# Optimization experiments

Measured on AMD Instinct MI355X. Metric: run time of the kernel, lower is better.

## Reference

```python
import jax, jax.numpy as jnp
import numpy as np

B, L, D = 16, 4096, 1024          # batch, query (latent) length, latent_dim
MODS = [("image", 2048), ("audio", 1024), ("text", 768)]


def setup_inputs() -> dict:
    key = jax.random.key(0)
    ks = iter(jax.random.split(key, 64))
    inp = {"S": jax.random.normal(next(ks), (B, L, D), jnp.float32)}
    for mod, din in MODS:
        inp[f"feat_{mod}"] = jax.random.normal(next(ks), (B, din), jnp.float32)
        # kv_proj: Linear(input_dim -> latent_dim)
        inp[f"Wkv_{mod}"] = jax.random.normal(next(ks), (D, din), jnp.float32) * (din ** -0.5)
        inp[f"bkv_{mod}"] = jnp.zeros((D,), jnp.float32)
        # MHA value projection (D -> D); k/q projections drop out because
        # softmax over a single key is identically 1 (exact, not approximate).
        inp[f"Wv_{mod}"] = jax.random.normal(next(ks), (D, D), jnp.float32) * (D ** -0.5)
        inp[f"bv_{mod}"] = jnp.zeros((D,), jnp.float32)
        # MHA out_proj (D -> D)
        inp[f"Wo_{mod}"] = jax.random.normal(next(ks), (D, D), jnp.float32) * (D ** -0.5)
        inp[f"bo_{mod}"] = jnp.zeros((D,), jnp.float32)
    return inp


def _modality_out(feat, Wkv, bkv, Wv, bv, Wo, bo):
    # kv_proj -> v_proj -> out_proj ; attention weights over 1 key are exactly 1,
    # so the MHA output is this vector broadcast over all L query positions.
    kv = feat @ Wkv.T + bkv        # [B, D]
    v = kv @ Wv.T + bv             # [B, D]
    return v @ Wo.T + bo           # [B, D]


def reference(S,
              feat_image, Wkv_image, bkv_image, Wv_image, bv_image, Wo_image, bo_image,
              feat_audio, Wkv_audio, bkv_audio, Wv_audio, bv_audio, Wo_audio, bo_audio,
              feat_text, Wkv_text, bkv_text, Wv_text, bv_text, Wo_text, bo_text):
    # Sequential residual adds S = S + out_mod commute; fuse into one add.
    delta = (_modality_out(feat_image, Wkv_image, bkv_image, Wv_image, bv_image, Wo_image, bo_image)
             + _modality_out(feat_audio, Wkv_audio, bkv_audio, Wv_audio, bv_audio, Wo_audio, bo_audio)
             + _modality_out(feat_text, Wkv_text, bkv_text, Wv_text, bv_text, Wo_text, bo_text))
    return S + delta[:, None, :]   # broadcast over query length L
```

## Files before the change

### kernel.cpp

```cpp
#include <hip/hip_runtime.h>


#define B_ 16
#define L_ 4096
#define D_ 1024

__global__ void gemv64(const float* __restrict__ x,
                       const float* __restrict__ W,
                       const float* __restrict__ bias,
                       float* __restrict__ y,
                       int K, int accumulate) {
    int wave = (blockIdx.x * blockDim.x + threadIdx.x) >> 6;
    int lane = threadIdx.x & 63;
    int b = wave >> 10;
    int d = wave & 1023;

    const float* xr = x + (size_t)b * K;
    const float* wr = W + (size_t)d * K;

    float sum = 0.f;
    for (int k = lane * 4; k < K; k += 256) {
        float4 xv = *(const float4*)(xr + k);
        float4 wv = *(const float4*)(wr + k);
        sum += xv.x * wv.x + xv.y * wv.y + xv.z * wv.z + xv.w * wv.w;
    }
    for (int off = 32; off; off >>= 1)
        sum += __shfl_xor(sum, off, 64);

    if (lane == 0) {
        float r = sum + bias[d];
        if (accumulate) y[wave] += r;
        else            y[wave]  = r;
    }
}

__global__ void add_bcast(const float4* __restrict__ S,
                          const float4* __restrict__ delta,
                          float4* __restrict__ out) {
    int i = blockIdx.x * blockDim.x + threadIdx.x;
    int b  = i >> 20;
    int d4 = i & 255;
    float4 s = S[i];
    float4 dl = delta[(b << 8) + d4];
    float4 r;
    r.x = s.x + dl.x;
    r.y = s.y + dl.y;
    r.z = s.z + dl.z;
    r.w = s.w + dl.w;
    out[i] = r;
}

extern "C" void kernel_launch(void* const* d_in, const int* in_sizes, int n_in,
                              void* d_out, int out_size, void* d_ws, size_t ws_size,
                              hipStream_t stream) {
    const float* S = (const float*)d_in[0];

    const int dins[3] = {2048, 1024, 768};
    const float *feat[3], *Wkv[3], *bkv[3], *Wv[3], *bv[3], *Wo[3], *bo[3];
    for (int m = 0; m < 3; ++m) {
        int base = 1 + m * 7;
        feat[m] = (const float*)d_in[base + 0];
        Wkv[m]  = (const float*)d_in[base + 1];
        bkv[m]  = (const float*)d_in[base + 2];
        Wv[m]   = (const float*)d_in[base + 3];
        bv[m]   = (const float*)d_in[base + 4];
        Wo[m]   = (const float*)d_in[base + 5];
        bo[m]   = (const float*)d_in[base + 6];
    }

    float* ws = (float*)d_ws;
    const int BD = B_ * D_;
    float* kv[3]  = {ws, ws + BD, ws + 2 * BD};
    float* v[3]   = {ws + 3 * BD, ws + 4 * BD, ws + 5 * BD};
    float* delta  = ws + 6 * BD;

    const int gemv_blocks = (BD * 64) / 256;
    const dim3 gb(gemv_blocks), tb(256);

    for (int m = 0; m < 3; ++m)
        gemv64<<<gb, tb, 0, stream>>>(feat[m], Wkv[m], bkv[m], kv[m], dins[m], 0);
    for (int m = 0; m < 3; ++m)
        gemv64<<<gb, tb, 0, stream>>>(kv[m], Wv[m], bv[m], v[m], D_, 0);
    for (int m = 0; m < 3; ++m)
        gemv64<<<gb, tb, 0, stream>>>(v[m], Wo[m], bo[m], delta, D_, m != 0);

    const int total4 = (B_ * L_ * D_) / 4;
    add_bcast<<<total4 / 256, 256, 0, stream>>>((const float4*)S,
                                                (const float4*)delta,
                                                (float4*)d_out);
}
```

Before: 545.7 us.

## Batch per-modality GEMVs into one launch per stage and stream the broadcast add

The three per-modality GEMVs of each stage are merged into a single launch indexed by modality, and the out-projection stage sums all three modalities inside one wave, so the read-modify-write accumulation into delta goes away. This cuts ten launches down to four. The broadcast add becomes a grid-stride loop with nontemporal loads and stores, meant to keep the streaming S traffic out of the cache. The total is dominated by the 256MB read plus 256MB write of S, so the achievable gain is limited to launch overhead and small GEMV costs.

```diff
diff --git a/kernel.cpp b/kernel.cpp
--- a/kernel.cpp
+++ b/kernel.cpp
@@ -5,18 +5,27 @@
 #define L_ 4096
 #define D_ 1024
 
-__global__ void gemv64(const float* __restrict__ x,
-                       const float* __restrict__ W,
-                       const float* __restrict__ bias,
-                       float* __restrict__ y,
-                       int K, int accumulate) {
-    int wave = (blockIdx.x * blockDim.x + threadIdx.x) >> 6;
+typedef float v4f __attribute__((ext_vector_type(4)));
+
+struct StageArgs {
+    const float* x[3];
+    const float* W[3];
+    const float* bias[3];
+    float*       y[3];
+    int          K[3];
+};
+
+__global__ __launch_bounds__(256) void gemv_stage(StageArgs a) {
+    int wid  = (blockIdx.x * 256 + threadIdx.x) >> 6;
     int lane = threadIdx.x & 63;
-    int b = wave >> 10;
-    int d = wave & 1023;
+    int m = wid >> 14;
+    int r = wid & 16383;
+    int bb = r >> 10;
+    int d  = r & 1023;
+    int K = a.K[m];
 
-    const float* xr = x + (size_t)b * K;
-    const float* wr = W + (size_t)d * K;
+    const float* xr = a.x[m] + bb * K;
+    const float* wr = a.W[m] + (size_t)d * K;
 
     float sum = 0.f;
     for (int k = lane * 4; k < K; k += 256) {
@@ -24,30 +33,56 @@
         float4 wv = *(const float4*)(wr + k);
         sum += xv.x * wv.x + xv.y * wv.y + xv.z * wv.z + xv.w * wv.w;
     }
-    for (int off = 32; off; off >>= 1)
-        sum += __shfl_xor(sum, off, 64);
+    for (int off = 32; off; off >>= 1) sum += __shfl_xor(sum, off, 64);
 
-    if (lane == 0) {
-        float r = sum + bias[d];
-        if (accumulate) y[wave] += r;
-        else            y[wave]  = r;
-    }
+    if (lane == 0) a.y[m][(bb << 10) + d] = sum + a.bias[m][d];
 }
 
-__global__ void add_bcast(const float4* __restrict__ S,
-                          const float4* __restrict__ delta,
-                          float4* __restrict__ out) {
-    int i = blockIdx.x * blockDim.x + threadIdx.x;
-    int b  = i >> 20;
-    int d4 = i & 255;
-    float4 s = S[i];
-    float4 dl = delta[(b << 8) + d4];
-    float4 r;
-    r.x = s.x + dl.x;
-    r.y = s.y + dl.y;
-    r.z = s.z + dl.z;
-    r.w = s.w + dl.w;
-    out[i] = r;
+struct Stage3Args {
+    const float* v0; const float* v1; const float* v2;
+    const float* W0; const float* W1; const float* W2;
+    const float* b0; const float* b1; const float* b2;
+    float* delta;
+};
+
+__global__ __launch_bounds__(256) void gemv_stage3(Stage3Args a) {
+    int wid  = (blockIdx.x * 256 + threadIdx.x) >> 6;
+    int lane = threadIdx.x & 63;
+    int bb = wid >> 10;
+    int d  = wid & 1023;
+
+    const float* xs[3] = { a.v0 + (bb << 10), a.v1 + (bb << 10), a.v2 + (bb << 10) };
+    const float* ws[3] = { a.W0 + ((size_t)d << 10), a.W1 + ((size_t)d << 10),
+                           a.W2 + ((size_t)d << 10) };
+    float sum = 0.f;
+    #pragma unroll
+    for (int m = 0; m < 3; ++m) {
+        const float* xr = xs[m];
+        const float* wr = ws[m];
+        #pragma unroll
+        for (int k = lane * 4; k < 1024; k += 256) {
+            float4 xv = *(const float4*)(xr + k);
+            float4 wv = *(const float4*)(wr + k);
+            sum += xv.x * wv.x + xv.y * wv.y + xv.z * wv.z + xv.w * wv.w;
+        }
+    }
+    for (int off = 32; off; off >>= 1) sum += __shfl_xor(sum, off, 64);
+
+    if (lane == 0)
+        a.delta[(bb << 10) + d] = sum + a.b0[d] + a.b1[d] + a.b2[d];
+}
+
+__global__ __launch_bounds__(256) void add_bcast(const v4f* __restrict__ S,
+                                                 const v4f* __restrict__ delta,
+                                                 v4f* __restrict__ out, int total4) {
+    int stride = gridDim.x * 256;
+    for (int i = blockIdx.x * 256 + threadIdx.x; i < total4; i += stride) {
+        int b  = i >> 20;
+        int d4 = i & 255;
+        v4f s  = __builtin_nontemporal_load(S + i);
+        v4f dl = delta[(b << 8) + d4];
+        __builtin_nontemporal_store(s + dl, out + i);
+    }
 }
 
 extern "C" void kernel_launch(void* const* d_in, const int* in_sizes, int n_in,
@@ -74,18 +109,24 @@
     float* v[3]   = {ws + 3 * BD, ws + 4 * BD, ws + 5 * BD};
     float* delta  = ws + 6 * BD;
 
-    const int gemv_blocks = (BD * 64) / 256;
-    const dim3 gb(gemv_blocks), tb(256);
+    StageArgs s1;
+    for (int m = 0; m < 3; ++m) {
+        s1.x[m] = feat[m]; s1.W[m] = Wkv[m]; s1.bias[m] = bkv[m];
+        s1.y[m] = kv[m];   s1.K[m] = dins[m];
+    }
+    gemv_stage<<<12288, 256, 0, stream>>>(s1);
 
-    for (int m = 0; m < 3; ++m)
-        gemv64<<<gb, tb, 0, stream>>>(feat[m], Wkv[m], bkv[m], kv[m], dins[m], 0);
-    for (int m = 0; m < 3; ++m)
-        gemv64<<<gb, tb, 0, stream>>>(kv[m], Wv[m], bv[m], v[m], D_, 0);
-    for (int m = 0; m < 3; ++m)
-        gemv64<<<gb, tb, 0, stream>>>(v[m], Wo[m], bo[m], delta, D_, m != 0);
+    StageArgs s2;
+    for (int m = 0; m < 3; ++m) {
+        s2.x[m] = kv[m]; s2.W[m] = Wv[m]; s2.bias[m] = bv[m];
+        s2.y[m] = v[m];  s2.K[m] = D_;
+    }
+    gemv_stage<<<12288, 256, 0, stream>>>(s2);
+
+    Stage3Args s3 = { v[0], v[1], v[2], Wo[0], Wo[1], Wo[2], bo[0], bo[1], bo[2], delta };
+    gemv_stage3<<<4096, 256, 0, stream>>>(s3);
 
     const int total4 = (B_ * L_ * D_) / 4;
-    add_bcast<<<total4 / 256, 256, 0, stream>>>((const float4*)S,
-                                                (const float4*)delta,
-                                                (float4*)d_out);
+    add_bcast<<<16384, 256, 0, stream>>>((const v4f*)S, (const v4f*)delta,
+                                         (v4f*)d_out, total4);
 }
```

After: 533.6 us. 1.02x faster.
